# Optimization experiments

Hardware: AMD Instinct MI355X
Metric: run time of the kernel (lower is better)

The kernel has to match this reference:

```python
import jax, jax.numpy as jnp
import numpy as np

S = 3      # SAMPLE_SIZE
U = 4      # UPSCALE
HID = 64


def _forward(x_in, sampler_w, sampler_b, w1, b1, w2, b2, w3, b3, w4, b4, w5, b5, w6, b6):
    B, C, H, W = x_in.shape  # C == 1
    Hp, Wp = H - (S - 1), W - (S - 1)
    # unfold: every 3x3 patch -> flattened vector of 9 (row-major i*3+j), matches F.unfold ordering
    img = x_in[:, 0]  # [B,H,W]
    patches = jnp.stack(
        [img[:, i:i + Hp, j:j + Wp] for i in range(S) for j in range(S)], axis=-1
    )  # [B,Hp,Wp,9]
    # AutoSample: softmax over the 9 taps per output channel, bias forced to zero
    wsamp = jax.nn.softmax(sampler_w.reshape(4, S * S), axis=1)  # [4,9]
    s = jnp.einsum('bhwk,ck->bhwc', patches, wsamp) + sampler_b * 0.0  # [B,Hp,Wp,4]
    # PixelShuffle(2) on [N,4,1,1] -> [N,1,2,2]: spatial (i,j) = channel i*2+j.
    # conv1 (2x2 kernel on 2x2 input) == dense over those 4 values; w1 is conv1.weight.reshape(64,4)
    x = jnp.einsum('bhwc,oc->bhwo', s, w1) + b1  # [B,Hp,Wp,64]
    # chain of 1x1 convs with ReLU before each
    for w, b in ((w2, b2), (w3, b3), (w4, b4), (w5, b5)):
        x = jnp.einsum('bhwi,oi->bhwo', jax.nn.relu(x), w) + b
    y = jnp.einsum('bhwi,oi->bhwo', jax.nn.relu(x), w6) + b6  # [B,Hp,Wp,16]
    # PixelShuffle(4) per patch + fold(stride=4): channel i*4+j -> output (h*4+i, w*4+j)
    y = y.reshape(B, Hp, Wp, U, U).transpose(0, 1, 3, 2, 4).reshape(B, 1, Hp * U, Wp * U)
    return y


def setup_inputs() -> dict:
    key = jax.random.key(0)
    ks = jax.random.split(key, 9)
    B, H, W = 16, 256, 256
    he4 = float(np.sqrt(2.0 / 4.0))
    he64 = float(np.sqrt(2.0 / 64.0))
    he9 = float(np.sqrt(2.0 / 9.0))
    return {
        'x_in': jax.random.normal(ks[0], (B, 1, H, W), jnp.float32),
        'sampler_w': jax.random.normal(ks[1], (4, 1, S, S), jnp.float32) * he9,
        'sampler_b': jnp.zeros((4,), jnp.float32),
        'w1': jax.random.normal(ks[2], (HID, 4), jnp.float32) * he4,
        'b1': jnp.zeros((HID,), jnp.float32),
        'w2': jax.random.normal(ks[3], (HID, HID), jnp.float32) * he64,
        'b2': jnp.zeros((HID,), jnp.float32),
        'w3': jax.random.normal(ks[4], (HID, HID), jnp.float32) * he64,
        'b3': jnp.zeros((HID,), jnp.float32),
        'w4': jax.random.normal(ks[5], (HID, HID), jnp.float32) * he64,
        'b4': jnp.zeros((HID,), jnp.float32),
        'w5': jax.random.normal(ks[6], (HID, HID), jnp.float32) * he64,
        'b5': jnp.zeros((HID,), jnp.float32),
        'w6': jax.random.normal(ks[7], (U * U, HID), jnp.float32) * he64,
        'b6': jnp.zeros((U * U,), jnp.float32),
    }


def reference(x_in, sampler_w, sampler_b, w1, b1, w2, b2, w3, b3, w4, b4, w5, b5, w6, b6):
    return _forward(x_in, sampler_w, sampler_b, w1, b1, w2, b2, w3, b3, w4, b4, w5, b5, w6, b6)
```

## Files before the change

kernel.cpp:

```cpp
#include <hip/hip_runtime.h>


typedef _Float16 f16x8  __attribute__((ext_vector_type(8)));
typedef _Float16 half2v __attribute__((ext_vector_type(2)));
typedef float    f32x16 __attribute__((ext_vector_type(16)));
typedef unsigned int u32;
typedef u32 u32x4 __attribute__((ext_vector_type(4)));

union FragU { f16x8 v; u32 w[4]; };

__device__ __forceinline__ u32 pkrne(float a, float b) {
    half2v h; h.x = (_Float16)a; h.y = (_Float16)b;
    return __builtin_bit_cast(u32, h);
}
__device__ __forceinline__ u32 pkrtz(float a, float b) {
    return __builtin_bit_cast(u32, __builtin_amdgcn_cvt_pkrtz(a, b));
}
__device__ __forceinline__ u32 pk_relu(u32 a) {
    half2v z = {};
    half2v r = __builtin_elementwise_max(__builtin_bit_cast(half2v, a), z);
    return __builtin_bit_cast(u32, r);
}

__device__ __forceinline__ f32x16 mfma16(const FragU& a, const FragU& b, f32x16 c) {
    return __builtin_amdgcn_mfma_f32_32x32x16_f16(a.v, b.v, c, 0, 0, 0);
}

__device__ __forceinline__ void pl32(u32& x, u32& y) {
    auto r = __builtin_amdgcn_permlane32_swap((int)x, (int)y, false, false);
    x = (u32)r[0]; y = (u32)r[1];
}

__device__ __forceinline__ void calc_coords(int g, int m, int& b, int& hp, int& wp) {
    unsigned P = (unsigned)(g * 32 + m);
    unsigned bb = P / 64516u;
    unsigned rem = P - bb * 64516u;
    unsigned h = rem / 254u;
    b = (int)bb; hp = (int)h; wp = (int)(rem - h * 254u);
}

__device__ __forceinline__ void prep_group(const float* __restrict__ x_in,
                                           int g, int m, int lo,
                                           float p[9], u32& ooff) {
    constexpr int OW = 1016;
    int b, hp, wp;
    calc_coords(g, m, b, hp, wp);
    const float* base = x_in + ((size_t)b << 16) + hp * 256 + wp;
#pragma unroll
    for (int i = 0; i < 3; ++i)
#pragma unroll
        for (int j = 0; j < 3; ++j)
            p[i * 3 + j] = base[i * 256 + j];
    ooff = (u32)b * (OW * OW) + (u32)(4 * hp + lo) * OW + 4 * wp;
}

__device__ __forceinline__ void epilogue(const f32x16& A0, const f32x16& A1,
                                         FragU (&B)[4]) {
    u32 ww[2][4][2];
#pragma unroll
    for (int mt = 0; mt < 2; ++mt) {
        const f32x16& A = mt ? A1 : A0;
#pragma unroll
        for (int q = 0; q < 4; ++q) {
            ww[mt][q][0] = pk_relu(pkrtz(A[4 * q + 0], A[4 * q + 1]));
            ww[mt][q][1] = pk_relu(pkrtz(A[4 * q + 2], A[4 * q + 3]));
        }
    }
#pragma unroll
    for (int ks = 0; ks < 4; ++ks) {
#pragma unroll
        for (int p = 0; p < 2; ++p) {
            u32 a = ww[ks >> 1][2 * (ks & 1) + 0][p];
            u32 b = ww[ks >> 1][2 * (ks & 1) + 1][p];
            pl32(a, b);
            B[ks].w[p]     = a;
            B[ks].w[p + 2] = b;
        }
    }
}

__device__ __forceinline__ void pack_B1(const float p[9], int lo, FragU& B1) {
    if (lo == 0) {
        B1.w[0] = pkrtz(p[0], p[1]);
        B1.w[1] = pkrtz(p[2], p[3]);
        B1.w[2] = pkrtz(p[4], p[5]);
        B1.w[3] = pkrtz(p[6], p[7]);
    } else {
        B1.w[0] = pkrtz(p[8], 1.0f);
        B1.w[1] = 0; B1.w[2] = 0; B1.w[3] = 0;
    }
}

__device__ __forceinline__ FragU lds_frag(const u32x4* wlds, int slot, int lane) {
    u32x4 v = wlds[slot * 64 + lane];
    FragU f;
    f.w[0] = v.x; f.w[1] = v.y; f.w[2] = v.z; f.w[3] = v.w;
    return f;
}

__device__ __forceinline__ FragU bias_frag(u32 w0) {
    FragU f;
    f.w[0] = w0; f.w[1] = 0; f.w[2] = 0; f.w[3] = 0;
    return f;
}

__global__ __launch_bounds__(256, 4) void srnet_mfma(
    const float* __restrict__ x_in,
    const float* __restrict__ sampler_w,
    const float* __restrict__ w1, const float* __restrict__ b1,
    const float* __restrict__ w2, const float* __restrict__ b2,
    const float* __restrict__ w3, const float* __restrict__ b3,
    const float* __restrict__ w4, const float* __restrict__ b4,
    const float* __restrict__ w5, const float* __restrict__ b5,
    const float* __restrict__ w6, const float* __restrict__ b6,
    float* __restrict__ out)
{
    constexpr int NG = 32258;
    constexpr int OW = 1016;

    const int lane = threadIdx.x & 63;
    const int m    = lane & 31;
    const int lo   = lane >> 5;

    __shared__ u32x4 wlds[38 * 64];

    const float* wptr[4] = { w2, w3, w4, w5 };
    for (int e = threadIdx.x; e < 2048; e += 256) {
        const int L  = e >> 9;
        const int f  = (e >> 6) & 7;
        const int l  = e & 63;
        const int mt = f >> 2, ks = f & 3;
        const float* src = wptr[L] + (32 * mt + (l & 31)) * 64 + 16 * ks + 8 * (l >> 5);
        const float4 f0 = *(const float4*)(src);
        const float4 f1 = *(const float4*)(src + 4);
        u32x4 v;
        v.x = pkrne(f0.x, f0.y); v.y = pkrne(f0.z, f0.w);
        v.z = pkrne(f1.x, f1.y); v.w = pkrne(f1.z, f1.w);
        wlds[(2 + L * 8 + f) * 64 + l] = v;
    }
    if (threadIdx.x < 64) {
        const int l = threadIdx.x, lm = l & 31, llo = l >> 5;
        const bool vr = (lm < 16);
        const int r6 = vr ? lm : 0;
#pragma unroll
        for (int ks = 0; ks < 4; ++ks) {
            const float* src = w6 + r6 * 64 + 16 * ks + 8 * llo;
            const float4 f0 = *(const float4*)(src);
            const float4 f1 = *(const float4*)(src + 4);
            u32x4 v;
            v.x = vr ? pkrne(f0.x, f0.y) : 0; v.y = vr ? pkrne(f0.z, f0.w) : 0;
            v.z = vr ? pkrne(f1.x, f1.y) : 0; v.w = vr ? pkrne(f1.z, f1.w) : 0;
            wlds[(34 + ks) * 64 + l] = v;
        }
    }
    if (threadIdx.x >= 64 && threadIdx.x < 128) {
        const int l = threadIdx.x - 64, lm = l & 31, llo = l >> 5;
        float ws[4][9];
#pragma unroll
        for (int c = 0; c < 4; ++c) {
            float mx = sampler_w[c * 9];
#pragma unroll
            for (int k = 1; k < 9; ++k) mx = fmaxf(mx, sampler_w[c * 9 + k]);
            float e[9]; float sum = 0.f;
#pragma unroll
            for (int k = 0; k < 9; ++k) { e[k] = __expf(sampler_w[c * 9 + k] - mx); sum += e[k]; }
            float inv = 1.f / sum;
#pragma unroll
            for (int k = 0; k < 9; ++k) ws[c][k] = e[k] * inv;
        }
#pragma unroll
        for (int mt = 0; mt < 2; ++mt) {
            const int row = 32 * mt + lm;
            const float4 wr = *(const float4*)(w1 + row * 4);
            float we[9];
#pragma unroll
            for (int k = 0; k < 9; ++k)
                we[k] = wr.x * ws[0][k] + wr.y * ws[1][k] + wr.z * ws[2][k] + wr.w * ws[3][k];
            u32x4 v;
            if (llo == 0) {
                v.x = pkrne(we[0], we[1]); v.y = pkrne(we[2], we[3]);
                v.z = pkrne(we[4], we[5]); v.w = pkrne(we[6], we[7]);
            } else {
                v.x = pkrne(we[8], b1[row]);
                v.y = 0; v.z = 0; v.w = 0;
            }
            wlds[mt * 64 + l] = v;
        }
    }
    __syncthreads();

    u32 bfr[8];
#pragma unroll
    for (int L = 0; L < 4; ++L) {
        const float* bsrc = (L == 0) ? b2 : (L == 1) ? b3 : (L == 2) ? b4 : b5;
#pragma unroll
        for (int mt = 0; mt < 2; ++mt)
            bfr[L * 2 + mt] = (lo == 0) ? pkrne(bsrc[32 * mt + m], 0.f) : 0u;
    }
    FragU B4;
    B4.w[0] = (lo == 0) ? pkrne(1.0f, 0.f) : 0u;
    B4.w[1] = 0; B4.w[2] = 0; B4.w[3] = 0;
    float b6r[8];
#pragma unroll
    for (int j = 0; j < 4; ++j) { b6r[j] = b6[4 * lo + j]; b6r[4 + j] = b6[8 + 4 * lo + j]; }
    const f32x16 z{};

    const int wid = (int)((blockIdx.x * blockDim.x + threadIdx.x) >> 6);
    const int nw  = (int)((gridDim.x * blockDim.x) >> 6);

    for (int g = wid; g < NG; g += nw) {
        asm volatile("" ::: "memory");

        float p[9];
        u32 oo;
        prep_group(x_in, g, m, lo, p, oo);

        FragU B1;
        pack_B1(p, lo, B1);

        f32x16 c0, c1;

        c0 = mfma16(lds_frag(wlds, 0, lane), B1, z);
        c1 = mfma16(lds_frag(wlds, 1, lane), B1, z);

        FragU B[4];
        epilogue(c0, c1, B);

#pragma unroll
        for (int L = 0; L < 4; ++L) {
            c0 = mfma16(bias_frag(bfr[L * 2 + 0]), B4, z);
            c1 = mfma16(bias_frag(bfr[L * 2 + 1]), B4, z);
#pragma unroll
            for (int ks = 0; ks < 4; ++ks) {
                c0 = mfma16(lds_frag(wlds, 2 + L * 8 + ks,     lane), B[ks], c0);
                c1 = mfma16(lds_frag(wlds, 2 + L * 8 + 4 + ks, lane), B[ks], c1);
            }
            epilogue(c0, c1, B);
        }

        c0 = mfma16(lds_frag(wlds, 34, lane), B[0], z);
#pragma unroll
        for (int ks = 1; ks < 4; ++ks)
            c0 = mfma16(lds_frag(wlds, 34 + ks, lane), B[ks], c0);

        float* obase = out + oo;
        *(float4*)(obase)          = make_float4(c0[0] + b6r[0], c0[1] + b6r[1],
                                                 c0[2] + b6r[2], c0[3] + b6r[3]);
        *(float4*)(obase + 2 * OW) = make_float4(c0[4] + b6r[4], c0[5] + b6r[5],
                                                 c0[6] + b6r[6], c0[7] + b6r[7]);
    }
}

extern "C" void kernel_launch(void* const* d_in, const int* in_sizes, int n_in,
                              void* d_out, int out_size, void* d_ws, size_t ws_size,
                              hipStream_t stream)
{
    const float* x_in      = (const float*)d_in[0];
    const float* sampler_w = (const float*)d_in[1];
    const float* w1 = (const float*)d_in[3];
    const float* b1 = (const float*)d_in[4];
    const float* w2 = (const float*)d_in[5];
    const float* b2 = (const float*)d_in[6];
    const float* w3 = (const float*)d_in[7];
    const float* b3 = (const float*)d_in[8];
    const float* w4 = (const float*)d_in[9];
    const float* b4 = (const float*)d_in[10];
    const float* w5 = (const float*)d_in[11];
    const float* b5 = (const float*)d_in[12];
    const float* w6 = (const float*)d_in[13];
    const float* b6 = (const float*)d_in[14];
    float* out = (float*)d_out;

    dim3 grid(1024);
    dim3 block(256);
    hipLaunchKernelGGL(srnet_mfma, grid, block, 0, stream,
                       x_in, sampler_w, w1, b1, w2, b2, w3, b3,
                       w4, b4, w5, b5, w6, b6, out);
}
```

Before: 53.77 us.

## Process two pixel groups per wave iteration to reuse LDS weight fragments

Each wave now handles a pair of 32-pixel groups per loop iteration, so every weight fragment read from LDS feeds two independent MFMA chains. This halves LDS weight traffic per pixel and gives the scheduler two interleaved MFMA dependency chains to hide latency. The grid is halved to 512 blocks and the launch bounds drop to one block per SM minimum, which lets register use grow but may reduce occupancy.

```diff
diff --git a/kernel.cpp b/kernel.cpp
--- a/kernel.cpp
+++ b/kernel.cpp
@@ -104,7 +104,7 @@
     return f;
 }
 
-__global__ __launch_bounds__(256, 4) void srnet_mfma(
+__global__ __launch_bounds__(256, 1) void srnet_mfma(
     const float* __restrict__ x_in,
     const float* __restrict__ sampler_w,
     const float* __restrict__ w1, const float* __restrict__ b1,
@@ -115,8 +115,8 @@
     const float* __restrict__ w6, const float* __restrict__ b6,
     float* __restrict__ out)
 {
-    constexpr int NG = 32258;
-    constexpr int OW = 1016;
+    constexpr int NPAIR = 16129;
+    constexpr int OW    = 1016;
 
     const int lane = threadIdx.x & 63;
     const int m    = lane & 31;
@@ -208,46 +208,78 @@
     const int wid = (int)((blockIdx.x * blockDim.x + threadIdx.x) >> 6);
     const int nw  = (int)((gridDim.x * blockDim.x) >> 6);
 
-    for (int g = wid; g < NG; g += nw) {
+    for (int pg = wid; pg < NPAIR; pg += nw) {
         asm volatile("" ::: "memory");
 
-        float p[9];
-        u32 oo;
-        prep_group(x_in, g, m, lo, p, oo);
-
-        FragU B1;
-        pack_B1(p, lo, B1);
-
-        f32x16 c0, c1;
-
-        c0 = mfma16(lds_frag(wlds, 0, lane), B1, z);
-        c1 = mfma16(lds_frag(wlds, 1, lane), B1, z);
-
-        FragU B[4];
-        epilogue(c0, c1, B);
+        float pa[9], pb[9];
+        u32 oa, ob;
+        prep_group(x_in, 2 * pg + 0, m, lo, pa, oa);
+        prep_group(x_in, 2 * pg + 1, m, lo, pb, ob);
+
+        FragU B1a, B1b;
+        pack_B1(pa, lo, B1a);
+        pack_B1(pb, lo, B1b);
+
+        f32x16 c0a, c1a, c0b, c1b;
+
+        {
+            FragU wA = lds_frag(wlds, 0, lane);
+            FragU wB = lds_frag(wlds, 1, lane);
+            c0a = mfma16(wA, B1a, z);
+            c0b = mfma16(wA, B1b, z);
+            c1a = mfma16(wB, B1a, z);
+            c1b = mfma16(wB, B1b, z);
+        }
+
+        FragU Ba[4], Bb[4];
+        epilogue(c0a, c1a, Ba);
+        epilogue(c0b, c1b, Bb);
 
 #pragma unroll
         for (int L = 0; L < 4; ++L) {
-            c0 = mfma16(bias_frag(bfr[L * 2 + 0]), B4, z);
-            c1 = mfma16(bias_frag(bfr[L * 2 + 1]), B4, z);
+            FragU bf0 = bias_frag(bfr[L * 2 + 0]);
+            FragU bf1 = bias_frag(bfr[L * 2 + 1]);
+            c0a = mfma16(bf0, B4, z);
+            c0b = mfma16(bf0, B4, z);
+            c1a = mfma16(bf1, B4, z);
+            c1b = mfma16(bf1, B4, z);
 #pragma unroll
             for (int ks = 0; ks < 4; ++ks) {
-                c0 = mfma16(lds_frag(wlds, 2 + L * 8 + ks,     lane), B[ks], c0);
-                c1 = mfma16(lds_frag(wlds, 2 + L * 8 + 4 + ks, lane), B[ks], c1);
+                FragU w0 = lds_frag(wlds, 2 + L * 8 + ks,     lane);
+                FragU w1l = lds_frag(wlds, 2 + L * 8 + 4 + ks, lane);
+                c0a = mfma16(w0,  Ba[ks], c0a);
+                c0b = mfma16(w0,  Bb[ks], c0b);
+                c1a = mfma16(w1l, Ba[ks], c1a);
+                c1b = mfma16(w1l, Bb[ks], c1b);
             }
-            epilogue(c0, c1, B);
-        }
-
-        c0 = mfma16(lds_frag(wlds, 34, lane), B[0], z);
-#pragma unroll
-        for (int ks = 1; ks < 4; ++ks)
-            c0 = mfma16(lds_frag(wlds, 34 + ks, lane), B[ks], c0);
-
-        float* obase = out + oo;
-        *(float4*)(obase)          = make_float4(c0[0] + b6r[0], c0[1] + b6r[1],
-                                                 c0[2] + b6r[2], c0[3] + b6r[3]);
-        *(float4*)(obase + 2 * OW) = make_float4(c0[4] + b6r[4], c0[5] + b6r[5],
-                                                 c0[6] + b6r[6], c0[7] + b6r[7]);
+            epilogue(c0a, c1a, Ba);
+            epilogue(c0b, c1b, Bb);
+        }
+
+        {
+            FragU w6f = lds_frag(wlds, 34, lane);
+            c0a = mfma16(w6f, Ba[0], z);
+            c0b = mfma16(w6f, Bb[0], z);
+        }
+#pragma unroll
+        for (int ks = 1; ks < 4; ++ks) {
+            FragU w6f = lds_frag(wlds, 34 + ks, lane);
+            c0a = mfma16(w6f, Ba[ks], c0a);
+            c0b = mfma16(w6f, Bb[ks], c0b);
+        }
+
+        {
+            float* obase = out + oa;
+            *(float4*)(obase)          = make_float4(c0a[0] + b6r[0], c0a[1] + b6r[1],
+                                                     c0a[2] + b6r[2], c0a[3] + b6r[3]);
+            *(float4*)(obase + 2 * OW) = make_float4(c0a[4] + b6r[4], c0a[5] + b6r[5],
+                                                     c0a[6] + b6r[6], c0a[7] + b6r[7]);
+            obase = out + ob;
+            *(float4*)(obase)          = make_float4(c0b[0] + b6r[0], c0b[1] + b6r[1],
+                                                     c0b[2] + b6r[2], c0b[3] + b6r[3]);
+            *(float4*)(obase + 2 * OW) = make_float4(c0b[4] + b6r[4], c0b[5] + b6r[5],
+                                                     c0b[6] + b6r[6], c0b[7] + b6r[7]);
+        }
     }
 }
 
@@ -271,7 +303,7 @@
     const float* b6 = (const float*)d_in[14];
     float* out = (float*)d_out;
 
-    dim3 grid(1024);
+    dim3 grid(512);
     dim3 block(256);
     hipLaunchKernelGGL(srnet_mfma, grid, block, 0, stream,
                        x_in, sampler_w, w1, b1, w2, b2, w3, b3,
```

Result: slower. 57.05 us (+6.1%).

## Prefetch next group inputs and keep layer-2/3 weights in registers

Applied to the files above, without the earlier changes.

Software-pipelines the grid-stride loop so the next group's input patch is loaded while the current group's MFMA chain runs. It also caches the 16 weight fragments for the first two hidden layers in registers instead of re-reading them from LDS each iteration. Launch bounds are relaxed to one block per SIMD hint and the grid is halved to fit the larger register footprint. This trades occupancy for latency hiding and fewer LDS reads.

```diff
diff --git a/kernel.cpp b/kernel.cpp
--- a/kernel.cpp
+++ b/kernel.cpp
@@ -104,7 +104,7 @@
     return f;
 }
 
-__global__ __launch_bounds__(256, 4) void srnet_mfma(
+__global__ __launch_bounds__(256, 1) void srnet_mfma(
     const float* __restrict__ x_in,
     const float* __restrict__ sampler_w,
     const float* __restrict__ w1, const float* __restrict__ b1,
@@ -189,6 +189,11 @@
     }
     __syncthreads();
 
+    FragU wreg[16];
+#pragma unroll
+    for (int f = 0; f < 16; ++f)
+        wreg[f] = lds_frag(wlds, 2 + f, lane);
+
     u32 bfr[8];
 #pragma unroll
     for (int L = 0; L < 4; ++L) {
@@ -208,16 +213,22 @@
     const int wid = (int)((blockIdx.x * blockDim.x + threadIdx.x) >> 6);
     const int nw  = (int)((gridDim.x * blockDim.x) >> 6);
 
-    for (int g = wid; g < NG; g += nw) {
+    int g = wid;
+    float p[9];
+    u32 oo = 0;
+    if (g < NG) prep_group(x_in, g, m, lo, p, oo);
+
+    while (g < NG) {
+        const int gn = g + nw;
         asm volatile("" ::: "memory");
-
-        float p[9];
-        u32 oo;
-        prep_group(x_in, g, m, lo, p, oo);
 
         FragU B1;
         pack_B1(p, lo, B1);
 
+        float pn[9];
+        u32 oon = 0;
+        if (gn < NG) prep_group(x_in, gn, m, lo, pn, oon);
+
         f32x16 c0, c1;
 
         c0 = mfma16(lds_frag(wlds, 0, lane), B1, z);
@@ -227,7 +238,19 @@
         epilogue(c0, c1, B);
 
 #pragma unroll
-        for (int L = 0; L < 4; ++L) {
+        for (int L = 0; L < 2; ++L) {
+            c0 = mfma16(bias_frag(bfr[L * 2 + 0]), B4, z);
+            c1 = mfma16(bias_frag(bfr[L * 2 + 1]), B4, z);
+#pragma unroll
+            for (int ks = 0; ks < 4; ++ks) {
+                c0 = mfma16(wreg[L * 8 + ks],     B[ks], c0);
+                c1 = mfma16(wreg[L * 8 + 4 + ks], B[ks], c1);
+            }
+            epilogue(c0, c1, B);
+        }
+
+#pragma unroll
+        for (int L = 2; L < 4; ++L) {
             c0 = mfma16(bias_frag(bfr[L * 2 + 0]), B4, z);
             c1 = mfma16(bias_frag(bfr[L * 2 + 1]), B4, z);
 #pragma unroll
@@ -248,6 +271,11 @@
                                                  c0[2] + b6r[2], c0[3] + b6r[3]);
         *(float4*)(obase + 2 * OW) = make_float4(c0[4] + b6r[4], c0[5] + b6r[5],
                                                  c0[6] + b6r[6], c0[7] + b6r[7]);
+
+        g = gn;
+        oo = oon;
+#pragma unroll
+        for (int k = 0; k < 9; ++k) p[k] = pn[k];
     }
 }
 
@@ -271,7 +299,7 @@
     const float* b6 = (const float*)d_in[14];
     float* out = (float*)d_out;
 
-    dim3 grid(1024);
+    dim3 grid(512);
     dim3 block(256);
     hipLaunchKernelGGL(srnet_mfma, grid, block, 0, stream,
                        x_in, sampler_w, w1, b1, w2, b2, w3, b3,
```

Result: slower. 58.36 us (+8.5%).
